# Kernel optimization log

Hardware: AMD Instinct MI355X
Metric: run time of the kernel (lower is better)

## Reference

```python
import jax, jax.numpy as jnp
import numpy as np

N_HEAD = 8
N_FEAT = 256
CHUNK = 64          # window/chunk size N
D_K = N_FEAT // N_HEAD
SCALE = D_K ** (-0.5)
B_ = 2048           # batch * nChunkNum
NCHUNK = 128        # nChunkNum (B_ % NCHUNK == 0)


def setup_inputs() -> dict:
    key = jax.random.key(0)
    ks = jax.random.split(key, 12)
    f32 = jnp.float32
    query = jax.random.normal(ks[0], (B_, CHUNK, N_FEAT), f32)
    key_t = jax.random.normal(ks[1], (B_, CHUNK, N_FEAT), f32)
    value = jax.random.normal(ks[2], (B_, CHUNK, N_FEAT), f32)
    # padding mask (B_, time2): multiplicative 0/1 floats
    mask = jax.random.randint(ks[3], (B_, CHUNK), 0, 2).astype(f32)
    # shifted-chunk additive mask (nChunkNum, N, N): 0 for neighbors, -100 otherwise
    cm_bin = jax.random.randint(ks[4], (NCHUNK, CHUNK, CHUNK), 0, 2)
    chunk_mask = jnp.where(cm_bin == 1, 0.0, -100.0).astype(f32)
    def lin(k):
        return jax.random.normal(k, (N_FEAT, N_FEAT), f32) * 0.02
    Wq, Wk, Wv, Wo = lin(ks[5]), lin(ks[6]), lin(ks[7]), lin(ks[8])
    bq = jnp.zeros((N_FEAT,), f32)
    bk = jnp.zeros((N_FEAT,), f32)
    bv = jnp.zeros((N_FEAT,), f32)
    bo = jnp.zeros((N_FEAT,), f32)
    rpb_table = jax.random.normal(ks[9], (2 * CHUNK - 1, N_HEAD), f32) * 0.02
    return {"query": query, "key": key_t, "value": value, "mask": mask,
            "chunk_mask": chunk_mask, "Wq": Wq, "bq": bq, "Wk": Wk, "bk": bk,
            "Wv": Wv, "bv": bv, "Wo": Wo, "bo": bo, "rpb_table": rpb_table}


def _rel_pos_index():
    # index[i, j] = (i - j) + CHUNK - 1, shape (N, N)
    w = jnp.arange(CHUNK)
    return w[:, None] - w[None, :] + (CHUNK - 1)


def reference(query, key, value, mask, chunk_mask, Wq, bq, Wk, bk, Wv, bv, Wo, bo, rpb_table):
    B, N, _ = query.shape
    # qkv projections -> (B, h, N, d_k)
    def proj(x, W, b):
        y = x @ W.T + b
        return y.reshape(B, N, N_HEAD, D_K).transpose(0, 2, 1, 3)
    q = proj(query, Wq, bq)
    k = proj(key, Wk, bk)
    v = proj(value, Wv, bv)
    # windowed attention scores (B, h, N, N)
    scores = jnp.einsum("bhid,bhjd->bhij", q, k) * SCALE
    # relative position bias: gather (N, N, h) -> (h, N, N)
    rpb = rpb_table[_rel_pos_index()].transpose(2, 0, 1)
    scores = scores + rpb[None]
    # padding mask: multiply, then fill zeros with -100 (as in torch source)
    scores = scores * mask[:, None, None, :]
    scores = jnp.where(scores == 0, jnp.float32(-100.0), scores)
    # additive shifted-chunk mask
    nC = chunk_mask.shape[0]
    scores = scores.reshape(B // nC, nC, N_HEAD, N, N) + chunk_mask[None, :, None]
    scores = scores.reshape(B, N_HEAD, N, N)
    attn = jax.nn.softmax(scores, axis=-1)
    x = jnp.einsum("bhij,bhjd->bhid", attn, v)          # (B, h, N, d_k)
    x = x.transpose(0, 2, 1, 3).reshape(B, N, N_FEAT)     # (B, N, n_feat)
    return x @ Wo.T + bo
```

## Files before the change

### kernel.cpp

```cpp
#include <hip/hip_runtime.h>
#include <hip/hip_bf16.h>

typedef __bf16 bf16_t;
typedef __bf16 bf16x8 __attribute__((ext_vector_type(8)));
typedef __bf16 bf16x4 __attribute__((ext_vector_type(4)));
typedef float f32x4 __attribute__((ext_vector_type(4)));

#define OFF_A   0
#define OFF_B   32768
#define OFF_RPB 65536
#define OFF_CMM (65536 + 4096)
#define OFF_PAD (65536 + 4096 + 512)
#define SMEM_BYTES (65536 + 4096 + 512 + 8)

__device__ __forceinline__ int tile_off(int r, int c) {
  return (r << 9) + ((((c >> 3) ^ (r & 7)) << 4) | ((c & 7) << 1));
}
__device__ __forceinline__ int vt_off(int d, int j) {
  return (d << 7) + ((((j >> 3) ^ (d & 7)) << 4) | ((j & 7) << 1));
}
__device__ __forceinline__ int ps_off(int i, int j) {
  return (i << 6) + ((((j >> 3) ^ ((i >> 1) & 3)) << 4) | ((j & 7) << 1));
}

template <int UNROLL>
__device__ __forceinline__ void stage_x(const float* __restrict__ src, char* __restrict__ dst, int tid) {
  const float4* s4 = (const float4*)src;
#pragma unroll
  for (int kk = 0; kk < 8; kk += UNROLL) {
    float4 v[UNROLL];
#pragma unroll
    for (int u = 0; u < UNROLL; ++u) v[u] = s4[tid + ((kk + u) << 9)];
#pragma unroll
    for (int u = 0; u < UNROLL; ++u) {
      int f = tid + ((kk + u) << 9);
      int row = f >> 6;
      int col = (f & 63) << 2;
      bf16x4 p;
      p[0] = (bf16_t)v[u].x; p[1] = (bf16_t)v[u].y; p[2] = (bf16_t)v[u].z; p[3] = (bf16_t)v[u].w;
      *(bf16x4*)(dst + tile_off(row, col)) = p;
    }
  }
}

__device__ __forceinline__ void gemm_tile(const char* __restrict__ sA, const bf16_t* __restrict__ W,
                                          int cb, int l15, int g, f32x4 acc[4][2]) {
#pragma unroll
  for (int kt = 0; kt < 8; ++kt) {
    bf16x8 a[4];
#pragma unroll
    for (int mt = 0; mt < 4; ++mt)
      a[mt] = *(const bf16x8*)(sA + tile_off(mt*16 + l15, kt*32 + g*8));
#pragma unroll
    for (int nt = 0; nt < 2; ++nt) {
      bf16x8 bw = *(const bf16x8*)(W + (cb + nt*16 + l15)*256 + kt*32 + g*8);
#pragma unroll
      for (int mt = 0; mt < 4; ++mt)
        acc[mt][nt] = __builtin_amdgcn_mfma_f32_16x16x32_bf16(a[mt], bw, acc[mt][nt], 0, 0, 0);
    }
  }
}

__global__ __launch_bounds__(512)
__attribute__((amdgpu_waves_per_eu(4, 4)))
void chunk_attn_kernel(
    const float* __restrict__ qg, const float* __restrict__ kg, const float* __restrict__ vg,
    const float* __restrict__ maskg, const float* __restrict__ cmg,
    const float* __restrict__ bq, const float* __restrict__ bk, const float* __restrict__ bv,
    const float* __restrict__ bo, const float* __restrict__ rpbg,
    const bf16_t* __restrict__ Wb, float* __restrict__ outg) {
  extern __shared__ char sm[];
  char*  bufA  = sm + OFF_A;
  char*  bufB  = sm + OFF_B;
  float* sRpb  = (float*)(sm + OFF_RPB);
  char*  sCmm  = sm + OFF_CMM;

  const int b = blockIdx.x, tid = threadIdx.x;
  const int wave = tid >> 6, lane = tid & 63, l15 = lane & 15, g = lane >> 4;
  const int cb = wave << 5;
  char* scr = bufB + (wave << 12);

  for (int i = tid; i < 1016; i += 512) sRpb[((i & 7) << 7) + (i >> 3)] = rpbg[i];
  {
    if (wave == 0) {
      float mv = maskg[(b << 6) + lane];
      unsigned long long bm = __ballot(mv == 0.0f);
      if (lane == 0) *(unsigned long long*)(sm + OFF_PAD) = bm;
    }
    const float* cmb = cmg + ((size_t)(b & 127) << 12);
#pragma unroll
    for (int it = 0; it < 8; ++it) {
      int row = (wave << 3) + it;
      float cv = cmb[(row << 6) + lane];
      unsigned long long bm = __ballot(cv < -50.0f);
      if (lane == 0) *(unsigned long long*)(sCmm + (row << 3)) = bm;
    }
  }
  stage_x<4>(qg + (size_t)b*16384, bufA, tid);
  stage_x<4>(kg + (size_t)b*16384, bufB, tid);
  __syncthreads();

  {
    f32x4 acc[4][2] = {};
    gemm_tile(bufA, Wb + 0*65536, cb, l15, g, acc);
    __syncthreads();
    float b0 = bq[cb+l15], b1 = bq[cb+16+l15];
#pragma unroll
    for (int mt = 0; mt < 4; ++mt)
#pragma unroll
      for (int nt = 0; nt < 2; ++nt)
#pragma unroll
        for (int r = 0; r < 4; ++r)
          *(bf16_t*)(bufA + tile_off(mt*16 + g*4 + r, cb + nt*16 + l15)) =
              (bf16_t)(acc[mt][nt][r] + (nt ? b1 : b0));
  }
  {
    f32x4 acc[4][2] = {};
    gemm_tile(bufB, Wb + 1*65536, cb, l15, g, acc);
    __syncthreads();
    float b0 = bk[cb+l15], b1 = bk[cb+16+l15];
#pragma unroll
    for (int mt = 0; mt < 4; ++mt)
#pragma unroll
      for (int nt = 0; nt < 2; ++nt)
#pragma unroll
        for (int r = 0; r < 4; ++r)
          *(bf16_t*)(bufB + tile_off(mt*16 + g*4 + r, cb + nt*16 + l15)) =
              (bf16_t)(acc[mt][nt][r] + (nt ? b1 : b0));
  }
  __asm__ volatile("s_waitcnt lgkmcnt(0)" ::: "memory");

  const float* rpbw = sRpb + (wave << 7);
  unsigned long long padm = *(const unsigned long long*)(sm + OFF_PAD);
  unsigned int padl = (unsigned int)padm, padh = (unsigned int)(padm >> 32);
  float rinv[4];
  bf16x4 pbf[4][4];
#pragma unroll
  for (int half = 0; half < 2; ++half) {
    f32x4 Sh[4][2];
    {
      bf16x8 qb0 = *(const bf16x8*)(bufA + tile_off((2*half + 0)*16 + l15, cb + g*8));
      bf16x8 qb1 = *(const bf16x8*)(bufA + tile_off((2*half + 1)*16 + l15, cb + g*8));
      const f32x4 z = {};
#pragma unroll
      for (int mj = 0; mj < 4; ++mj) {
        bf16x8 ka = *(const bf16x8*)(bufB + tile_off(mj*16 + l15, cb + g*8));
        Sh[mj][0] = __builtin_amdgcn_mfma_f32_16x16x32_bf16(ka, qb0, z, 0, 0, 0);
        Sh[mj][1] = __builtin_amdgcn_mfma_f32_16x16x32_bf16(ka, qb1, z, 0, 0, 0);
      }
    }
#pragma unroll
    for (int nih = 0; nih < 2; ++nih) {
      int ni = 2*half + nih;
      int i = ni*16 + l15;
      unsigned long long cmm = *(const unsigned long long*)(sCmm + (i << 3));
      unsigned int cml = (unsigned int)cmm, cmh = (unsigned int)(cmm >> 32);
      float m = -1e30f;
#pragma unroll
      for (int mj = 0; mj < 4; ++mj) {
        unsigned int cw = (mj >= 2) ? cmh : cml;
        unsigned int pw = (mj >= 2) ? padh : padl;
#pragma unroll
        for (int r = 0; r < 4; ++r) {
          int j = mj*16 + g*4 + r;
          int sh = j & 31;
          float s1 = Sh[mj][nih][r] * 0.17677669529663689f + rpbw[i - j + 63];
          float base = ((pw >> sh) & 1u) ? -100.0f : s1;
          float sc = ((cw >> sh) & 1u) ? base - 100.0f : base;
          Sh[mj][nih][r] = sc;
          m = fmaxf(m, sc);
        }
      }
      m = fmaxf(m, __shfl_xor(m, 16));
      m = fmaxf(m, __shfl_xor(m, 32));
      float s = 0.0f;
#pragma unroll
      for (int mj = 0; mj < 4; ++mj)
#pragma unroll
        for (int r = 0; r < 4; ++r) {
          float p = __expf(Sh[mj][nih][r] - m);
          pbf[mj][ni][r] = (bf16_t)p;
          s += p;
        }
      s += __shfl_xor(s, 16);
      s += __shfl_xor(s, 32);
      rinv[ni] = 1.0f / s;
    }
  }

  __syncthreads();
  stage_x<2>(vg + (size_t)b*16384, bufB, tid);
  __syncthreads();

  {
    f32x4 vacc[4][2] = {};
    gemm_tile(bufB, Wb + 2*65536, cb, l15, g, vacc);
    float b0 = bv[cb+l15], b1 = bv[cb+16+l15];
#pragma unroll
    for (int nt = 0; nt < 2; ++nt)
#pragma unroll
      for (int mt = 0; mt < 4; ++mt) {
        bf16x4 p;
#pragma unroll
        for (int r = 0; r < 4; ++r) p[r] = (bf16_t)(vacc[mt][nt][r] + (nt ? b1 : b0));
        *(bf16x4*)(bufA + vt_off(cb + nt*16 + l15, mt*16 + g*4)) = p;
      }
  }
  __syncthreads();

  f32x4 Xa[2][4] = {};
#pragma unroll
  for (int h2 = 0; h2 < 2; ++h2) {
#pragma unroll
    for (int mj = 2*h2; mj < 2*h2 + 2; ++mj)
#pragma unroll
      for (int ni = 0; ni < 4; ++ni)
        *(bf16x4*)(scr + ps_off(ni*16 + l15, (mj & 1)*16 + g*4)) = pbf[mj][ni];
    __asm__ volatile("s_waitcnt lgkmcnt(0)" ::: "memory");
    bf16x8 va[2], pb[4];
#pragma unroll
    for (int mtd = 0; mtd < 2; ++mtd)
      va[mtd] = *(const bf16x8*)(bufA + vt_off(cb + mtd*16 + l15, h2*32 + g*8));
#pragma unroll
    for (int ni = 0; ni < 4; ++ni)
      pb[ni] = *(const bf16x8*)(scr + ps_off(ni*16 + l15, g*8));
#pragma unroll
    for (int mtd = 0; mtd < 2; ++mtd)
#pragma unroll
      for (int ni = 0; ni < 4; ++ni)
        Xa[mtd][ni] = __builtin_amdgcn_mfma_f32_16x16x32_bf16(va[mtd], pb[ni], Xa[mtd][ni], 0, 0, 0);
  }

  __syncthreads();
#pragma unroll
  for (int mtd = 0; mtd < 2; ++mtd)
#pragma unroll
    for (int ni = 0; ni < 4; ++ni)
#pragma unroll
      for (int r = 0; r < 4; ++r) {
        int dloc = mtd*16 + g*4 + r;
        int i = ni*16 + l15;
        *(bf16_t*)(bufB + tile_off(i, cb + dloc)) = (bf16_t)(Xa[mtd][ni][r] * rinv[ni]);
      }
  __syncthreads();

  {
    f32x4 acc[4][2] = {};
    gemm_tile(bufB, Wb + 3*65536, cb, l15, g, acc);
    float b0 = bo[cb+l15], b1 = bo[cb+16+l15];
    float* ob = outg + (size_t)b * 16384;
#pragma unroll
    for (int mt = 0; mt < 4; ++mt)
#pragma unroll
      for (int nt = 0; nt < 2; ++nt)
#pragma unroll
        for (int r = 0; r < 4; ++r)
          ob[(mt*16 + g*4 + r)*256 + cb + nt*16 + l15] = acc[mt][nt][r] + (nt ? b1 : b0);
  }
}

__global__ void cvt_weights(const float* __restrict__ Wq, const float* __restrict__ Wk,
                            const float* __restrict__ Wv, const float* __restrict__ Wo,
                            bf16_t* __restrict__ dst) {
  int idx = blockIdx.x * 256 + threadIdx.x;
  int which = idx >> 14;
  int off = idx & 16383;
  const float* src = (which == 0) ? Wq : (which == 1) ? Wk : (which == 2) ? Wv : Wo;
  float4 v = ((const float4*)src)[off];
  bf16x4 p;
  p[0] = (bf16_t)v.x; p[1] = (bf16_t)v.y; p[2] = (bf16_t)v.z; p[3] = (bf16_t)v.w;
  *(bf16x4*)(dst + which*65536 + off*4) = p;
}

extern "C" void kernel_launch(void* const* d_in, const int* in_sizes, int n_in,
                              void* d_out, int out_size, void* d_ws, size_t ws_size,
                              hipStream_t stream) {
  (void)in_sizes; (void)n_in; (void)out_size; (void)ws_size;
  const float* qg  = (const float*)d_in[0];
  const float* kg  = (const float*)d_in[1];
  const float* vg  = (const float*)d_in[2];
  const float* mg  = (const float*)d_in[3];
  const float* cmg = (const float*)d_in[4];
  const float* Wq  = (const float*)d_in[5];
  const float* bq  = (const float*)d_in[6];
  const float* Wk  = (const float*)d_in[7];
  const float* bk  = (const float*)d_in[8];
  const float* Wv  = (const float*)d_in[9];
  const float* bv  = (const float*)d_in[10];
  const float* Wo  = (const float*)d_in[11];
  const float* bo  = (const float*)d_in[12];
  const float* rpb = (const float*)d_in[13];
  bf16_t* Wb = (bf16_t*)d_ws;
  float* outg = (float*)d_out;

  hipFuncSetAttribute(reinterpret_cast<const void*>(chunk_attn_kernel),
                      hipFuncAttributeMaxDynamicSharedMemorySize, SMEM_BYTES);
  cvt_weights<<<256, 256, 0, stream>>>(Wq, Wk, Wv, Wo, Wb);
  chunk_attn_kernel<<<2048, 512, SMEM_BYTES, stream>>>(qg, kg, vg, mg, cmg,
      bq, bk, bv, bo, rpb, Wb, outg);
}
```

Baseline: 282.9 us.

## Stage P scratch in per-wave columns of bufB and drop redundant barriers

The softmax probabilities are now written into a layout where each wave owns a column slice of bufB (pk_off), which overlaps the head's own output-tile region. V is staged into bufA instead of bufB. The first half of P is written before the V projection, and the second half is written after the first PV MFMA pass. This lets the barrier before the PV product and the one before the output write-back be replaced by local lgkmcnt waits. The cost is an extra barrier after the V gemm, plus a buffer-aliasing scheme whose correctness depends on careful per-wave ownership.

```diff
diff --git a/kernel.cpp b/kernel.cpp
--- a/kernel.cpp
+++ b/kernel.cpp
@@ -19,8 +19,8 @@
 __device__ __forceinline__ int vt_off(int d, int j) {
   return (d << 7) + ((((j >> 3) ^ (d & 7)) << 4) | ((j & 7) << 1));
 }
-__device__ __forceinline__ int ps_off(int i, int j) {
-  return (i << 6) + ((((j >> 3) ^ ((i >> 1) & 3)) << 4) | ((j & 7) << 1));
+__device__ __forceinline__ int pk_off(int wv, int i, int t, int byteoff) {
+  return (i << 9) + ((((wv << 2) + t) ^ (i & 7)) << 4) + byteoff;
 }
 
 template <int UNROLL>
@@ -78,7 +78,6 @@
   const int b = blockIdx.x, tid = threadIdx.x;
   const int wave = tid >> 6, lane = tid & 63, l15 = lane & 15, g = lane >> 4;
   const int cb = wave << 5;
-  char* scr = bufB + (wave << 12);
 
   for (int i = tid; i < 1016; i += 512) sRpb[((i & 7) << 7) + (i >> 3)] = rpbg[i];
   {
@@ -134,7 +133,8 @@
   unsigned long long padm = *(const unsigned long long*)(sm + OFF_PAD);
   unsigned int padl = (unsigned int)padm, padh = (unsigned int)(padm >> 32);
   float rinv[4];
-  bf16x4 pbf[4][4];
+  bf16x4 pbf01[2][4];
+  bf16x4 pbf23[2][4];
 #pragma unroll
   for (int half = 0; half < 2; ++half) {
     f32x4 Sh[4][2];
@@ -179,7 +179,8 @@
 #pragma unroll
         for (int r = 0; r < 4; ++r) {
           float p = __expf(Sh[mj][nih][r] - m);
-          pbf[mj][ni][r] = (bf16_t)p;
+          if (mj < 2) pbf01[mj][ni][r] = (bf16_t)p;
+          else        pbf23[mj-2][ni][r] = (bf16_t)p;
           s += p;
         }
       s += __shfl_xor(s, 16);
@@ -188,13 +189,20 @@
     }
   }
 
-  __syncthreads();
-  stage_x<2>(vg + (size_t)b*16384, bufB, tid);
-  __syncthreads();
-
-  {
-    f32x4 vacc[4][2] = {};
-    gemm_tile(bufB, Wb + 2*65536, cb, l15, g, vacc);
+#pragma unroll
+  for (int mj = 0; mj < 2; ++mj)
+#pragma unroll
+    for (int ni = 0; ni < 4; ++ni)
+      *(bf16x4*)(bufB + pk_off(wave, ni*16 + l15, 2*mj + (g >> 1), (g & 1)*8)) = pbf01[mj][ni];
+
+  __syncthreads();
+  stage_x<2>(vg + (size_t)b*16384, bufA, tid);
+  __syncthreads();
+
+  f32x4 vacc[4][2] = {};
+  gemm_tile(bufA, Wb + 2*65536, cb, l15, g, vacc);
+  __syncthreads();
+  {
     float b0 = bv[cb+l15], b1 = bv[cb+16+l15];
 #pragma unroll
     for (int nt = 0; nt < 2; ++nt)
@@ -206,42 +214,44 @@
         *(bf16x4*)(bufA + vt_off(cb + nt*16 + l15, mt*16 + g*4)) = p;
       }
   }
-  __syncthreads();
+  __asm__ volatile("s_waitcnt lgkmcnt(0)" ::: "memory");
 
   f32x4 Xa[2][4] = {};
-#pragma unroll
-  for (int h2 = 0; h2 < 2; ++h2) {
-#pragma unroll
-    for (int mj = 2*h2; mj < 2*h2 + 2; ++mj)
-#pragma unroll
-      for (int ni = 0; ni < 4; ++ni)
-        *(bf16x4*)(scr + ps_off(ni*16 + l15, (mj & 1)*16 + g*4)) = pbf[mj][ni];
-    __asm__ volatile("s_waitcnt lgkmcnt(0)" ::: "memory");
-    bf16x8 va[2], pb[4];
-#pragma unroll
-    for (int mtd = 0; mtd < 2; ++mtd)
-      va[mtd] = *(const bf16x8*)(bufA + vt_off(cb + mtd*16 + l15, h2*32 + g*8));
+  {
+    bf16x8 va0 = *(const bf16x8*)(bufA + vt_off(cb + l15,      g*8));
+    bf16x8 va1 = *(const bf16x8*)(bufA + vt_off(cb + 16 + l15, g*8));
+#pragma unroll
+    for (int ni = 0; ni < 4; ++ni) {
+      bf16x8 pb = *(const bf16x8*)(bufB + pk_off(wave, ni*16 + l15, g, 0));
+      Xa[0][ni] = __builtin_amdgcn_mfma_f32_16x16x32_bf16(va0, pb, Xa[0][ni], 0, 0, 0);
+      Xa[1][ni] = __builtin_amdgcn_mfma_f32_16x16x32_bf16(va1, pb, Xa[1][ni], 0, 0, 0);
+    }
+  }
+#pragma unroll
+  for (int mj = 0; mj < 2; ++mj)
 #pragma unroll
     for (int ni = 0; ni < 4; ++ni)
-      pb[ni] = *(const bf16x8*)(scr + ps_off(ni*16 + l15, g*8));
-#pragma unroll
-    for (int mtd = 0; mtd < 2; ++mtd)
-#pragma unroll
-      for (int ni = 0; ni < 4; ++ni)
-        Xa[mtd][ni] = __builtin_amdgcn_mfma_f32_16x16x32_bf16(va[mtd], pb[ni], Xa[mtd][ni], 0, 0, 0);
-  }
-
-  __syncthreads();
+      *(bf16x4*)(bufB + pk_off(wave, ni*16 + l15, 2*mj + (g >> 1), (g & 1)*8)) = pbf23[mj][ni];
+  __asm__ volatile("s_waitcnt lgkmcnt(0)" ::: "memory");
+  {
+    bf16x8 va0 = *(const bf16x8*)(bufA + vt_off(cb + l15,      32 + g*8));
+    bf16x8 va1 = *(const bf16x8*)(bufA + vt_off(cb + 16 + l15, 32 + g*8));
+#pragma unroll
+    for (int ni = 0; ni < 4; ++ni) {
+      bf16x8 pb = *(const bf16x8*)(bufB + pk_off(wave, ni*16 + l15, g, 0));
+      Xa[0][ni] = __builtin_amdgcn_mfma_f32_16x16x32_bf16(va0, pb, Xa[0][ni], 0, 0, 0);
+      Xa[1][ni] = __builtin_amdgcn_mfma_f32_16x16x32_bf16(va1, pb, Xa[1][ni], 0, 0, 0);
+    }
+  }
+
 #pragma unroll
   for (int mtd = 0; mtd < 2; ++mtd)
 #pragma unroll
     for (int ni = 0; ni < 4; ++ni)
 #pragma unroll
-      for (int r = 0; r < 4; ++r) {
-        int dloc = mtd*16 + g*4 + r;
-        int i = ni*16 + l15;
-        *(bf16_t*)(bufB + tile_off(i, cb + dloc)) = (bf16_t)(Xa[mtd][ni][r] * rinv[ni]);
-      }
+      for (int r = 0; r < 4; ++r)
+        *(bf16_t*)(bufB + tile_off(ni*16 + l15, cb + mtd*16 + g*4 + r)) =
+            (bf16_t)(Xa[mtd][ni][r] * rinv[ni]);
   __syncthreads();
 
   {
```

New measurement: 291.4 us. 1.03x slower.

## Fuse Q and K projection GEMMs and compute all scores at once

Applied to the files above, without the earlier changes.

Merges the separate Q and K projection GEMM loops into one interleaved loop with two accumulator sets, so the MFMA chains are independent and share one barrier and one epilogue. Computes the full 64x64 score tile in a single pass instead of two halves, and changes the V staging unroll. Launch bounds go from a fixed 4 waves per EU to (512, 2), which lets the compiler use more registers. The aim is more instruction-level parallelism and fewer barriers, in exchange for higher register pressure and possible spills or lower occupancy.

```diff
diff --git a/kernel.cpp b/kernel.cpp
--- a/kernel.cpp
+++ b/kernel.cpp
@@ -61,8 +61,34 @@
   }
 }
 
-__global__ __launch_bounds__(512)
-__attribute__((amdgpu_waves_per_eu(4, 4)))
+__device__ __forceinline__ void gemm_tile2(const char* __restrict__ sA, const char* __restrict__ sB,
+                                           const bf16_t* __restrict__ W0, const bf16_t* __restrict__ W1,
+                                           int cb, int l15, int g,
+                                           f32x4 acc0[4][2], f32x4 acc1[4][2]) {
+  const bf16_t* w0p = W0 + (cb + l15)*256 + g*8;
+  const bf16_t* w1p = W1 + (cb + l15)*256 + g*8;
+#pragma unroll
+  for (int kt = 0; kt < 8; ++kt) {
+    bf16x8 a0[4], a1[4];
+#pragma unroll
+    for (int mt = 0; mt < 4; ++mt) {
+      a0[mt] = *(const bf16x8*)(sA + tile_off(mt*16 + l15, kt*32 + g*8));
+      a1[mt] = *(const bf16x8*)(sB + tile_off(mt*16 + l15, kt*32 + g*8));
+    }
+#pragma unroll
+    for (int nt = 0; nt < 2; ++nt) {
+      bf16x8 bw0 = *(const bf16x8*)(w0p + nt*16*256 + kt*32);
+      bf16x8 bw1 = *(const bf16x8*)(w1p + nt*16*256 + kt*32);
+#pragma unroll
+      for (int mt = 0; mt < 4; ++mt) {
+        acc0[mt][nt] = __builtin_amdgcn_mfma_f32_16x16x32_bf16(a0[mt], bw0, acc0[mt][nt], 0, 0, 0);
+        acc1[mt][nt] = __builtin_amdgcn_mfma_f32_16x16x32_bf16(a1[mt], bw1, acc1[mt][nt], 0, 0, 0);
+      }
+    }
+  }
+}
+
+__global__ __launch_bounds__(512, 2)
 void chunk_attn_kernel(
     const float* __restrict__ qg, const float* __restrict__ kg, const float* __restrict__ vg,
     const float* __restrict__ maskg, const float* __restrict__ cmg,
@@ -101,95 +127,89 @@
   __syncthreads();
 
   {
-    f32x4 acc[4][2] = {};
-    gemm_tile(bufA, Wb + 0*65536, cb, l15, g, acc);
+    f32x4 qacc[4][2] = {}, kacc[4][2] = {};
+    gemm_tile2(bufA, bufB, Wb + 0*65536, Wb + 1*65536, cb, l15, g, qacc, kacc);
     __syncthreads();
-    float b0 = bq[cb+l15], b1 = bq[cb+16+l15];
+    float bq0 = bq[cb+l15], bq1 = bq[cb+16+l15];
+    float bk0 = bk[cb+l15], bk1 = bk[cb+16+l15];
 #pragma unroll
     for (int mt = 0; mt < 4; ++mt)
 #pragma unroll
       for (int nt = 0; nt < 2; ++nt)
 #pragma unroll
-        for (int r = 0; r < 4; ++r)
-          *(bf16_t*)(bufA + tile_off(mt*16 + g*4 + r, cb + nt*16 + l15)) =
-              (bf16_t)(acc[mt][nt][r] + (nt ? b1 : b0));
-  }
-  {
-    f32x4 acc[4][2] = {};
-    gemm_tile(bufB, Wb + 1*65536, cb, l15, g, acc);
-    __syncthreads();
-    float b0 = bk[cb+l15], b1 = bk[cb+16+l15];
-#pragma unroll
-    for (int mt = 0; mt < 4; ++mt)
-#pragma unroll
-      for (int nt = 0; nt < 2; ++nt)
-#pragma unroll
-        for (int r = 0; r < 4; ++r)
-          *(bf16_t*)(bufB + tile_off(mt*16 + g*4 + r, cb + nt*16 + l15)) =
-              (bf16_t)(acc[mt][nt][r] + (nt ? b1 : b0));
+        for (int r = 0; r < 4; ++r) {
+          int row = mt*16 + g*4 + r, col = cb + nt*16 + l15;
+          *(bf16_t*)(bufA + tile_off(row, col)) = (bf16_t)(qacc[mt][nt][r] + (nt ? bq1 : bq0));
+          *(bf16_t*)(bufB + tile_off(row, col)) = (bf16_t)(kacc[mt][nt][r] + (nt ? bk1 : bk0));
+        }
   }
   __asm__ volatile("s_waitcnt lgkmcnt(0)" ::: "memory");
+
+  f32x4 St[4][4];
+  {
+    bf16x8 ka[4], qb[4];
+#pragma unroll
+    for (int t = 0; t < 4; ++t) {
+      ka[t] = *(const bf16x8*)(bufB + tile_off(t*16 + l15, cb + g*8));
+      qb[t] = *(const bf16x8*)(bufA + tile_off(t*16 + l15, cb + g*8));
+    }
+    const f32x4 z = {};
+#pragma unroll
+    for (int mj = 0; mj < 4; ++mj)
+#pragma unroll
+      for (int ni = 0; ni < 4; ++ni)
+        St[mj][ni] = __builtin_amdgcn_mfma_f32_16x16x32_bf16(ka[mj], qb[ni], z, 0, 0, 0);
+  }
 
   const float* rpbw = sRpb + (wave << 7);
   unsigned long long padm = *(const unsigned long long*)(sm + OFF_PAD);
   unsigned int padl = (unsigned int)padm, padh = (unsigned int)(padm >> 32);
+#pragma unroll
+  for (int mj = 0; mj < 4; ++mj) {
+    unsigned int pw = (mj >= 2) ? padh : padl;
+#pragma unroll
+    for (int ni = 0; ni < 4; ++ni) {
+      int i = ni*16 + l15;
+      unsigned long long cmm = *(const unsigned long long*)(sCmm + (i << 3));
+      unsigned int cw = (mj >= 2) ? (unsigned int)(cmm >> 32) : (unsigned int)cmm;
+#pragma unroll
+      for (int r = 0; r < 4; ++r) {
+        int j = mj*16 + g*4 + r;
+        int sh = j & 31;
+        float s1 = St[mj][ni][r] * 0.17677669529663689f + rpbw[i - j + 63];
+        float base = ((pw >> sh) & 1u) ? -100.0f : s1;
+        St[mj][ni][r] = ((cw >> sh) & 1u) ? base - 100.0f : base;
+      }
+    }
+  }
+
   float rinv[4];
   bf16x4 pbf[4][4];
 #pragma unroll
-  for (int half = 0; half < 2; ++half) {
-    f32x4 Sh[4][2];
-    {
-      bf16x8 qb0 = *(const bf16x8*)(bufA + tile_off((2*half + 0)*16 + l15, cb + g*8));
-      bf16x8 qb1 = *(const bf16x8*)(bufA + tile_off((2*half + 1)*16 + l15, cb + g*8));
-      const f32x4 z = {};
-#pragma unroll
-      for (int mj = 0; mj < 4; ++mj) {
-        bf16x8 ka = *(const bf16x8*)(bufB + tile_off(mj*16 + l15, cb + g*8));
-        Sh[mj][0] = __builtin_amdgcn_mfma_f32_16x16x32_bf16(ka, qb0, z, 0, 0, 0);
-        Sh[mj][1] = __builtin_amdgcn_mfma_f32_16x16x32_bf16(ka, qb1, z, 0, 0, 0);
-      }
-    }
-#pragma unroll
-    for (int nih = 0; nih < 2; ++nih) {
-      int ni = 2*half + nih;
-      int i = ni*16 + l15;
-      unsigned long long cmm = *(const unsigned long long*)(sCmm + (i << 3));
-      unsigned int cml = (unsigned int)cmm, cmh = (unsigned int)(cmm >> 32);
-      float m = -1e30f;
-#pragma unroll
-      for (int mj = 0; mj < 4; ++mj) {
-        unsigned int cw = (mj >= 2) ? cmh : cml;
-        unsigned int pw = (mj >= 2) ? padh : padl;
-#pragma unroll
-        for (int r = 0; r < 4; ++r) {
-          int j = mj*16 + g*4 + r;
-          int sh = j & 31;
-          float s1 = Sh[mj][nih][r] * 0.17677669529663689f + rpbw[i - j + 63];
-          float base = ((pw >> sh) & 1u) ? -100.0f : s1;
-          float sc = ((cw >> sh) & 1u) ? base - 100.0f : base;
-          Sh[mj][nih][r] = sc;
-          m = fmaxf(m, sc);
-        }
-      }
-      m = fmaxf(m, __shfl_xor(m, 16));
-      m = fmaxf(m, __shfl_xor(m, 32));
-      float s = 0.0f;
-#pragma unroll
-      for (int mj = 0; mj < 4; ++mj)
-#pragma unroll
-        for (int r = 0; r < 4; ++r) {
-          float p = __expf(Sh[mj][nih][r] - m);
-          pbf[mj][ni][r] = (bf16_t)p;
-          s += p;
-        }
-      s += __shfl_xor(s, 16);
-      s += __shfl_xor(s, 32);
-      rinv[ni] = 1.0f / s;
-    }
-  }
-
-  __syncthreads();
-  stage_x<2>(vg + (size_t)b*16384, bufB, tid);
+  for (int ni = 0; ni < 4; ++ni) {
+    float m = -1e30f;
+#pragma unroll
+    for (int mj = 0; mj < 4; ++mj)
+#pragma unroll
+      for (int r = 0; r < 4; ++r) m = fmaxf(m, St[mj][ni][r]);
+    m = fmaxf(m, __shfl_xor(m, 16));
+    m = fmaxf(m, __shfl_xor(m, 32));
+    float s = 0.0f;
+#pragma unroll
+    for (int mj = 0; mj < 4; ++mj)
+#pragma unroll
+      for (int r = 0; r < 4; ++r) {
+        float p = __expf(St[mj][ni][r] - m);
+        pbf[mj][ni][r] = (bf16_t)p;
+        s += p;
+      }
+    s += __shfl_xor(s, 16);
+    s += __shfl_xor(s, 32);
+    rinv[ni] = 1.0f / s;
+  }
+
+  __syncthreads();
+  stage_x<4>(vg + (size_t)b*16384, bufB, tid);
   __syncthreads();
 
   {
```

Result: faster. 251.8 us (-11.0%).
